# Kernel tuning notes

Measured on AMD Instinct MI355X. Metric: run time of the kernel, lower is better.

The kernel has to match this reference:

```python
import jax, jax.numpy as jnp
import numpy as np

SIZE = 65536
MAX_EDGES = 16777216  # n_edges = min(0.1*SIZE^2, MAX_EDGES) = MAX_EDGES, so all edges active


def setup_inputs() -> dict:
    key = jax.random.key(0)
    k1, k2, k3, k4 = jax.random.split(key, 4)
    x = jax.random.normal(k1, (SIZE,), dtype=jnp.float32)
    edge_weights = jax.random.normal(k2, (MAX_EDGES,), dtype=jnp.float32) * (2.0 / SIZE) ** 0.5
    bias = jnp.zeros((SIZE,), dtype=jnp.float32)
    src = jax.random.randint(k3, (MAX_EDGES,), 0, SIZE, dtype=jnp.int64 if jax.config.jax_enable_x64 else jnp.int32)
    dst = jax.random.randint(k4, (MAX_EDGES,), 0, SIZE, dtype=jnp.int64 if jax.config.jax_enable_x64 else jnp.int32)
    return {"x": x, "edge_weights": edge_weights, "bias": bias, "src": src, "dst": dst}


def reference(x, edge_weights, bias, src, dst):
    # gather -> elementwise multiply -> scatter_add -> + bias
    weighted = x[src] * edge_weights                    # [E]
    out = jax.ops.segment_sum(weighted, dst, num_segments=SIZE)  # [size]
    return out + bias
```

## Files before the change

kernel.cpp:

```cpp
#include <hip/hip_runtime.h>


#define NNODES  65536
#define NEDGES  16777216
#define RANGES  2
#define BINS    (NNODES / RANGES)
#define THREADS 1024
#define NCOPIES 128
#define GROUPS  16
#define CPG     (NCOPIES / GROUPS)

__global__ __launch_bounds__(THREADS, 4) void hist_kernel(
    const float* __restrict__ x,
    const float* __restrict__ w,
    const int*   __restrict__ src,
    const int*   __restrict__ dst,
    float*       __restrict__ ws,
    int B)
{
    extern __shared__ float h[];

    const int b = blockIdx.x;
    int r, c;
    if (B == NCOPIES) {
        r = (b >> 3) & (RANGES - 1);
        c = (b & 7) | ((b >> 4) << 3);
    } else {
        r = b & (RANGES - 1);
        c = b >> 1;
    }
    const int lo = r * BINS;

    for (int i = threadIdx.x; i < BINS; i += THREADS) h[i] = 0.0f;
    __syncthreads();

    const int4*   src4 = (const int4*)src;
    const int4*   dst4 = (const int4*)dst;
    const float4* wgt4 = (const float4*)w;

    const int n8     = NEDGES / 8;
    const int stride = B * THREADS;
    int g = c * THREADS + (int)threadIdx.x;

    if ((n8 % (2 * stride)) == 0 && n8 >= 2 * stride) {
        const int niter2 = n8 / (2 * stride);
        for (int it = 0; it < niter2; ++it, g += 2 * stride) {
            const int ga = g;
            const int gb = g + stride;

            int4   sA0 = src4[2 * ga], sA1 = src4[2 * ga + 1];
            int4   sB0 = src4[2 * gb], sB1 = src4[2 * gb + 1];
            int4   dA0 = dst4[2 * ga], dA1 = dst4[2 * ga + 1];
            int4   dB0 = dst4[2 * gb], dB1 = dst4[2 * gb + 1];
            float4 wA0 = wgt4[2 * ga], wA1 = wgt4[2 * ga + 1];
            float4 wB0 = wgt4[2 * gb], wB1 = wgt4[2 * gb + 1];

            int s[16] = { sA0.x, sA0.y, sA0.z, sA0.w,
                          sA1.x, sA1.y, sA1.z, sA1.w,
                          sB0.x, sB0.y, sB0.z, sB0.w,
                          sB1.x, sB1.y, sB1.z, sB1.w };
            unsigned bin[16] = {
                (unsigned)(dA0.x - lo), (unsigned)(dA0.y - lo),
                (unsigned)(dA0.z - lo), (unsigned)(dA0.w - lo),
                (unsigned)(dA1.x - lo), (unsigned)(dA1.y - lo),
                (unsigned)(dA1.z - lo), (unsigned)(dA1.w - lo),
                (unsigned)(dB0.x - lo), (unsigned)(dB0.y - lo),
                (unsigned)(dB0.z - lo), (unsigned)(dB0.w - lo),
                (unsigned)(dB1.x - lo), (unsigned)(dB1.y - lo),
                (unsigned)(dB1.z - lo), (unsigned)(dB1.w - lo) };
            float wv[16] = { wA0.x, wA0.y, wA0.z, wA0.w,
                             wA1.x, wA1.y, wA1.z, wA1.w,
                             wB0.x, wB0.y, wB0.z, wB0.w,
                             wB1.x, wB1.y, wB1.z, wB1.w };

            float v[16];
            #pragma unroll
            for (int k = 0; k < 16; ++k) {
                v[k] = 0.0f;
                if (bin[k] < (unsigned)BINS) v[k] = x[s[k]] * wv[k];
            }
            #pragma unroll
            for (int k = 0; k < 16; ++k) {
                if (bin[k] < (unsigned)BINS) atomicAdd(&h[bin[k]], v[k]);
            }
        }
    } else {
        for (; g < n8; g += stride) {
            int4   sa = src4[2 * g], sb = src4[2 * g + 1];
            int4   da = dst4[2 * g], db = dst4[2 * g + 1];
            float4 wa = wgt4[2 * g], wb = wgt4[2 * g + 1];

            int      s[8]  = { sa.x, sa.y, sa.z, sa.w, sb.x, sb.y, sb.z, sb.w };
            unsigned bin[8] = {
                (unsigned)(da.x - lo), (unsigned)(da.y - lo),
                (unsigned)(da.z - lo), (unsigned)(da.w - lo),
                (unsigned)(db.x - lo), (unsigned)(db.y - lo),
                (unsigned)(db.z - lo), (unsigned)(db.w - lo) };
            float    wv[8] = { wa.x, wa.y, wa.z, wa.w, wb.x, wb.y, wb.z, wb.w };

            float v[8];
            #pragma unroll
            for (int k = 0; k < 8; ++k) {
                v[k] = 0.0f;
                if (bin[k] < (unsigned)BINS) v[k] = x[s[k]] * wv[k];
            }
            #pragma unroll
            for (int k = 0; k < 8; ++k) {
                if (bin[k] < (unsigned)BINS) atomicAdd(&h[bin[k]], v[k]);
            }
        }
    }
    __syncthreads();

    float* outc = ws + (size_t)c * NNODES + lo;
    for (int i = threadIdx.x; i < BINS; i += THREADS) outc[i] = h[i];
}

__global__ __launch_bounds__(256) void reduceA_kernel(float* __restrict__ ws)
{
    const int NB = NNODES / (256 * 4);
    int g  = blockIdx.x / NB;
    int jb = blockIdx.x % NB;
    int i4 = jb * 256 + (int)threadIdx.x;

    float4* w4 = (float4*)ws;
    const int stride4 = NNODES / 4;

    float4 acc = w4[(size_t)(g * CPG) * stride4 + i4];
    #pragma unroll
    for (int cc = 1; cc < CPG; ++cc) {
        float4 t = w4[(size_t)(g * CPG + cc) * stride4 + i4];
        acc.x += t.x; acc.y += t.y; acc.z += t.z; acc.w += t.w;
    }
    w4[(size_t)(g * CPG) * stride4 + i4] = acc;
}

__global__ __launch_bounds__(256) void reduceB_kernel(
    const float* __restrict__ ws,
    const float* __restrict__ bias,
    float*       __restrict__ out)
{
    int i4 = blockIdx.x * 256 + (int)threadIdx.x;
    const float4* w4 = (const float4*)ws;
    const int stride4 = NNODES / 4;

    float4 acc = ((const float4*)bias)[i4];
    #pragma unroll
    for (int g = 0; g < GROUPS; ++g) {
        float4 t = w4[(size_t)(g * CPG) * stride4 + i4];
        acc.x += t.x; acc.y += t.y; acc.z += t.z; acc.w += t.w;
    }
    ((float4*)out)[i4] = acc;
}

__global__ __launch_bounds__(256) void reduce_generic_kernel(
    const float* __restrict__ ws,
    const float* __restrict__ bias,
    float*       __restrict__ out,
    int B)
{
    int i = blockIdx.x * 256 + (int)threadIdx.x;
    float acc = bias[i];
    for (int cc = 0; cc < B; ++cc) acc += ws[(size_t)cc * NNODES + i];
    out[i] = acc;
}

__global__ __launch_bounds__(256) void init_out_kernel(
    const float* __restrict__ bias, float* __restrict__ out)
{
    int i = blockIdx.x * blockDim.x + threadIdx.x;
    if (i < NNODES) out[i] = bias[i];
}

__global__ __launch_bounds__(256) void edge_atomic_kernel(
    const float* __restrict__ x, const float* __restrict__ w,
    const int* __restrict__ src, const int* __restrict__ dst,
    float* __restrict__ out)
{
    const int n4 = NEDGES / 4;
    int tid = blockIdx.x * blockDim.x + threadIdx.x;
    int stride = gridDim.x * blockDim.x;
    for (int i = tid; i < n4; i += stride) {
        int4 s = ((const int4*)src)[i];
        int4 d = ((const int4*)dst)[i];
        float4 ww = ((const float4*)w)[i];
        atomicAdd(&out[d.x], x[s.x] * ww.x);
        atomicAdd(&out[d.y], x[s.y] * ww.y);
        atomicAdd(&out[d.z], x[s.z] * ww.z);
        atomicAdd(&out[d.w], x[s.w] * ww.w);
    }
}

extern "C" void kernel_launch(void* const* d_in, const int* in_sizes, int n_in,
                              void* d_out, int out_size, void* d_ws, size_t ws_size,
                              hipStream_t stream) {
    const float* x    = (const float*)d_in[0];
    const float* w    = (const float*)d_in[1];
    const float* bias = (const float*)d_in[2];
    const int*   src  = (const int*)d_in[3];
    const int*   dst  = (const int*)d_in[4];
    float* out = (float*)d_out;
    float* ws  = (float*)d_ws;

    size_t copies = ws_size / ((size_t)NNODES * sizeof(float));
    int B = (int)(copies < NCOPIES ? copies : NCOPIES);

    if (B >= 1) {
        hist_kernel<<<B * RANGES, THREADS, BINS * sizeof(float), stream>>>(
            x, w, src, dst, ws, B);
        if (B == NCOPIES) {
            reduceA_kernel<<<GROUPS * (NNODES / 1024), 256, 0, stream>>>(ws);
            reduceB_kernel<<<NNODES / 1024, 256, 0, stream>>>(ws, bias, out);
        } else {
            reduce_generic_kernel<<<NNODES / 256, 256, 0, stream>>>(ws, bias, out, B);
        }
    } else {
        init_out_kernel<<<NNODES / 256, 256, 0, stream>>>(bias, out);
        edge_atomic_kernel<<<4096, 256, 0, stream>>>(x, w, src, dst, out);
    }
}
```

Before: 265.1 us.

## Precompute gathered products then histogram with four destination ranges

Adds a pass that computes x[src]*w once per edge into workspace (fp32, or fp16 if space is short), then a histogram kernel that reads only dst and the precomputed products, using 4 destination ranges with smaller shared-memory bins. It is meant to remove the repeated random gather of x and the repeated reads of src/w across range passes, and to shrink LDS per block for occupancy. In exchange it adds a 64MB write/read round trip, and more range passes re-read dst. The fp16 fallback loses precision.

New measurement: 328.6 us. +23.9%, slower.

```diff
diff --git a/kernel.cpp b/kernel.cpp
--- a/kernel.cpp
+++ b/kernel.cpp
@@ -3,12 +3,117 @@
 
 #define NNODES  65536
 #define NEDGES  16777216
-#define RANGES  2
-#define BINS    (NNODES / RANGES)
 #define THREADS 1024
 #define NCOPIES 128
 #define GROUPS  16
 #define CPG     (NCOPIES / GROUPS)
+
+#define RANGES  2
+#define BINS    (NNODES / RANGES)
+#define RANGES2 4
+#define BINS2   (NNODES / RANGES2)
+
+template <bool HALF>
+__global__ __launch_bounds__(256) void wx_kernel(
+    const float* __restrict__ x,
+    const float* __restrict__ w,
+    const int*   __restrict__ src,
+    void*        __restrict__ wxv)
+{
+    const int n8 = NEDGES / 8;
+    const int gs = gridDim.x * 256;
+    for (int i = blockIdx.x * 256 + (int)threadIdx.x; i < n8; i += gs) {
+        int4   s0 = ((const int4*)src)[2 * i];
+        int4   s1 = ((const int4*)src)[2 * i + 1];
+        float4 w0 = ((const float4*)w)[2 * i];
+        float4 w1 = ((const float4*)w)[2 * i + 1];
+        float v[8] = { x[s0.x] * w0.x, x[s0.y] * w0.y,
+                       x[s0.z] * w0.z, x[s0.w] * w0.w,
+                       x[s1.x] * w1.x, x[s1.y] * w1.y,
+                       x[s1.z] * w1.z, x[s1.w] * w1.w };
+        if constexpr (HALF) {
+            union { _Float16 h[8]; int4 p; } u;
+            #pragma unroll
+            for (int k = 0; k < 8; ++k) u.h[k] = (_Float16)v[k];
+            ((int4*)wxv)[i] = u.p;
+        } else {
+            float4 o0 = { v[0], v[1], v[2], v[3] };
+            float4 o1 = { v[4], v[5], v[6], v[7] };
+            ((float4*)wxv)[2 * i]     = o0;
+            ((float4*)wxv)[2 * i + 1] = o1;
+        }
+    }
+}
+
+template <bool HALF>
+__global__ __launch_bounds__(THREADS, 8) void hist2_kernel(
+    const int*  __restrict__ dst,
+    const void* __restrict__ wxv,
+    float*      __restrict__ ws)
+{
+    extern __shared__ float h[];
+
+    const int b  = blockIdx.x;
+    const int r  = (b >> 3) & (RANGES2 - 1);
+    const int c  = (b & 7) | ((b >> 5) << 3);
+    const int lo = r * BINS2;
+
+    for (int i = threadIdx.x; i < BINS2; i += THREADS) h[i] = 0.0f;
+    __syncthreads();
+
+    const int4* dst4 = (const int4*)dst;
+    const int   n8     = NEDGES / 8;
+    const int   stride = NCOPIES * THREADS;
+    int g = c * THREADS + (int)threadIdx.x;
+
+    const int niter2 = n8 / (2 * stride);
+    for (int it = 0; it < niter2; ++it, g += 2 * stride) {
+        const int ga = g;
+        const int gb = g + stride;
+
+        int4 dA0 = dst4[2 * ga], dA1 = dst4[2 * ga + 1];
+        int4 dB0 = dst4[2 * gb], dB1 = dst4[2 * gb + 1];
+
+        float vv[16];
+        if constexpr (HALF) {
+            int4 pa = ((const int4*)wxv)[ga];
+            int4 pb = ((const int4*)wxv)[gb];
+            union { int4 p; _Float16 h[8]; } ua, ub;
+            ua.p = pa; ub.p = pb;
+            #pragma unroll
+            for (int k = 0; k < 8; ++k) {
+                vv[k]     = (float)ua.h[k];
+                vv[8 + k] = (float)ub.h[k];
+            }
+        } else {
+            const float4* wx4 = (const float4*)wxv;
+            float4 wA0 = wx4[2 * ga], wA1 = wx4[2 * ga + 1];
+            float4 wB0 = wx4[2 * gb], wB1 = wx4[2 * gb + 1];
+            vv[0]=wA0.x; vv[1]=wA0.y; vv[2]=wA0.z; vv[3]=wA0.w;
+            vv[4]=wA1.x; vv[5]=wA1.y; vv[6]=wA1.z; vv[7]=wA1.w;
+            vv[8]=wB0.x; vv[9]=wB0.y; vv[10]=wB0.z; vv[11]=wB0.w;
+            vv[12]=wB1.x; vv[13]=wB1.y; vv[14]=wB1.z; vv[15]=wB1.w;
+        }
+
+        unsigned bin[16] = {
+            (unsigned)(dA0.x - lo), (unsigned)(dA0.y - lo),
+            (unsigned)(dA0.z - lo), (unsigned)(dA0.w - lo),
+            (unsigned)(dA1.x - lo), (unsigned)(dA1.y - lo),
+            (unsigned)(dA1.z - lo), (unsigned)(dA1.w - lo),
+            (unsigned)(dB0.x - lo), (unsigned)(dB0.y - lo),
+            (unsigned)(dB0.z - lo), (unsigned)(dB0.w - lo),
+            (unsigned)(dB1.x - lo), (unsigned)(dB1.y - lo),
+            (unsigned)(dB1.z - lo), (unsigned)(dB1.w - lo) };
+
+        #pragma unroll
+        for (int k = 0; k < 16; ++k)
+            if (bin[k] < (unsigned)BINS2) atomicAdd(&h[bin[k]], vv[k]);
+    }
+
+    __syncthreads();
+    float* outc = ws + (size_t)c * NNODES + lo;
+    for (int i = threadIdx.x; i < BINS2; i += THREADS) outc[i] = h[i];
+}
 
 __global__ __launch_bounds__(THREADS, 4) void hist_kernel(
     const float* __restrict__ x,
@@ -202,20 +307,37 @@
     float* out = (float*)d_out;
     float* ws  = (float*)d_ws;
 
-    size_t copies = ws_size / ((size_t)NNODES * sizeof(float));
-    int B = (int)(copies < NCOPIES ? copies : NCOPIES);
-
-    if (B >= 1) {
-        hist_kernel<<<B * RANGES, THREADS, BINS * sizeof(float), stream>>>(
-            x, w, src, dst, ws, B);
-        if (B == NCOPIES) {
-            reduceA_kernel<<<GROUPS * (NNODES / 1024), 256, 0, stream>>>(ws);
-            reduceB_kernel<<<NNODES / 1024, 256, 0, stream>>>(ws, bias, out);
+    const size_t copiesBytes = (size_t)NCOPIES * NNODES * sizeof(float);
+
+    if (ws_size >= copiesBytes + (size_t)NEDGES * sizeof(float)) {
+        void* wx = (void*)((char*)d_ws + copiesBytes);
+        wx_kernel<false><<<2048, 256, 0, stream>>>(x, w, src, wx);
+        hist2_kernel<false><<<NCOPIES * RANGES2, THREADS,
+                              BINS2 * sizeof(float), stream>>>(dst, wx, ws);
+        reduceA_kernel<<<GROUPS * (NNODES / 1024), 256, 0, stream>>>(ws);
+        reduceB_kernel<<<NNODES / 1024, 256, 0, stream>>>(ws, bias, out);
+    } else if (ws_size >= copiesBytes + (size_t)NEDGES * 2) {
+        void* wx = (void*)((char*)d_ws + copiesBytes);
+        wx_kernel<true><<<2048, 256, 0, stream>>>(x, w, src, wx);
+        hist2_kernel<true><<<NCOPIES * RANGES2, THREADS,
+                             BINS2 * sizeof(float), stream>>>(dst, wx, ws);
+        reduceA_kernel<<<GROUPS * (NNODES / 1024), 256, 0, stream>>>(ws);
+        reduceB_kernel<<<NNODES / 1024, 256, 0, stream>>>(ws, bias, out);
+    } else {
+        size_t copies = ws_size / ((size_t)NNODES * sizeof(float));
+        int B = (int)(copies < NCOPIES ? copies : NCOPIES);
+        if (B >= 1) {
+            hist_kernel<<<B * RANGES, THREADS, BINS * sizeof(float), stream>>>(
+                x, w, src, dst, ws, B);
+            if (B == NCOPIES) {
+                reduceA_kernel<<<GROUPS * (NNODES / 1024), 256, 0, stream>>>(ws);
+                reduceB_kernel<<<NNODES / 1024, 256, 0, stream>>>(ws, bias, out);
+            } else {
+                reduce_generic_kernel<<<NNODES / 256, 256, 0, stream>>>(ws, bias, out, B);
+            }
         } else {
-            reduce_generic_kernel<<<NNODES / 256, 256, 0, stream>>>(ws, bias, out, B);
-        }
-    } else {
-        init_out_kernel<<<NNODES / 256, 256, 0, stream>>>(bias, out);
-        edge_atomic_kernel<<<4096, 256, 0, stream>>>(x, w, src, dst, out);
-    }
-}
+            init_out_kernel<<<NNODES / 256, 256, 0, stream>>>(bias, out);
+            edge_atomic_kernel<<<4096, 256, 0, stream>>>(x, w, src, dst, out);
+        }
+    }
+}
```
